# Performance work log

Measured on AMD Instinct MI355X. Metric: run time of the kernel, lower is better.

The kernel has to match this reference:

```python
import jax, jax.numpy as jnp
import numpy as np

EPS = 1e-5
S = 192  # seq_len = 24*8
D = 512
DFF = 2048


def setup_inputs() -> dict:
    key = jax.random.key(0)
    ks = jax.random.split(key, 8)
    tgt = jax.random.normal(ks[0], (64, 24, 8, D), jnp.float32)
    memory = jax.random.normal(ks[1], (64, 24, 8, D), jnp.float32)
    W1 = jax.random.normal(ks[2], (D, D), jnp.float32) * 0.02
    b1 = jnp.zeros((D,), jnp.float32)
    se = jax.random.normal(ks[3], (S, S), jnp.float32)
    score_embed = (se + se.T).reshape(1, 1, S, S)
    W2 = jax.random.normal(ks[4], (DFF, S), jnp.float32) * 0.05
    b2 = jnp.zeros((DFF,), jnp.float32)
    W3 = jax.random.normal(ks[5], (1, DFF), jnp.float32) * 0.02
    b3 = jnp.zeros((1,), jnp.float32)
    return {
        'tgt': tgt, 'memory': memory,
        'W1': W1, 'b1': b1, 'score_embed': score_embed,
        'g1': jnp.ones((1,), jnp.float32), 'be1': jnp.zeros((1,), jnp.float32),
        'W2': W2, 'b2': b2,
        'g2': jnp.ones((DFF,), jnp.float32), 'be2': jnp.zeros((DFF,), jnp.float32),
        'W3': W3, 'b3': b3,
        'g3': jnp.ones((1,), jnp.float32), 'be3': jnp.zeros((1,), jnp.float32),
    }


def _bn(x, gamma, beta, axes):
    # BatchNorm in training mode: biased variance over `axes`.
    mean = jnp.mean(x, axis=axes, keepdims=True)
    var = jnp.mean((x - mean) ** 2, axis=axes, keepdims=True)
    return gamma * (x - mean) * jax.lax.rsqrt(var + EPS) + beta


def reference(tgt, memory, W1, b1, score_embed, g1, be1, W2, b2, g2, be2, W3, b3, g3, be3):
    q = tgt.shape[0]
    k = memory.shape[0]
    d = tgt.shape[-1]
    tgt = tgt.reshape(q, S, d)      # [q, t, d]
    memory = memory.reshape(k, S, d)  # [k, s, d]
    query = tgt @ W1.T + b1
    key = memory @ W1.T + b1
    # bilinear score with learned symmetric bias: [q, k, s, t]
    score = jnp.einsum('qtd,ksd->qkst', query, key) * jax.nn.sigmoid(score_embed)
    score = score.reshape(q * k, S, S)
    # dual-axis max pooling, concat -> [q*k, 2S]
    score = jnp.concatenate((score.max(axis=1), score.max(axis=2)), axis=-1)
    x = score.reshape(-1, 1, S)                       # [2qk, 1, S]
    x = _bn(x, g1.reshape(1, 1, 1), be1.reshape(1, 1, 1), (0, 2)).reshape(-1, S)
    x = x @ W2.T + b2                                 # [2qk, DFF]
    x = _bn(x, g2, be2, (0,))
    x = jax.nn.relu(x)
    x = x @ W3.T + b3                                 # [2qk, 1]
    x = x.reshape(-1, 2).sum(axis=-1, keepdims=True)  # [qk, 1]
    x = _bn(x, g3, be3, (0,))
    return x.reshape(q, k)
```

## Files before the change

kernel.cpp:

```cpp
#include <hip/hip_runtime.h>

#define SS 192
#define DD 512
#define DFF 2048
#define NROW 12288
#define EPSV 1e-5f

using bf16x8 = __attribute__((ext_vector_type(8))) __bf16;
using f32x4  = __attribute__((ext_vector_type(4))) float;

__device__ inline unsigned short f2bf(float f) {
    unsigned u = __float_as_uint(f);
    unsigned r = (u + 0x7FFFu + ((u >> 16) & 1u)) >> 16;
    return (unsigned short)r;
}
__device__ inline float bf2f(unsigned short h) {
    return __uint_as_float(((unsigned)h) << 16);
}
__device__ inline unsigned f2mono(float f) {
    unsigned u = __float_as_uint(f);
    return u ^ ((unsigned)((int)u >> 31) | 0x80000000u);
}
__device__ inline float mono2f(unsigned u) {
    unsigned b = (u & 0x80000000u) ? (u ^ 0x80000000u) : ~u;
    return __uint_as_float(b);
}
#define ENC_NEGINF 0x007FFFFFu

#define GLL16(g, l) __builtin_amdgcn_global_load_lds( \
    (const __attribute__((address_space(1))) void*)(g), \
    (__attribute__((address_space(3))) void*)(l), 16, 0, 0)

template<int NW>
__device__ inline float blockReduceSum(float v) {
    __shared__ float red[NW];
    #pragma unroll
    for (int o = 32; o > 0; o >>= 1) v += __shfl_down(v, o);
    int w = threadIdx.x >> 6;
    __syncthreads();
    if ((threadIdx.x & 63) == 0) red[w] = v;
    __syncthreads();
    if (threadIdx.x == 0) {
        float t = 0;
        #pragma unroll
        for (int i = 0; i < NW; i++) t += red[i];
        red[0] = t;
    }
    __syncthreads();
    return red[0];
}

__global__ void k_cvt(const float* __restrict__ src, unsigned short* __restrict__ dst) {
    int i = blockIdx.x * 256 + threadIdx.x;
    float4 v = ((const float4*)src)[i];
    unsigned short o[4] = { f2bf(v.x), f2bf(v.y), f2bf(v.z), f2bf(v.w) };
    ((uint2*)dst)[i] = *(uint2*)o;
}

__global__ void k_sig(const float* __restrict__ se, float* __restrict__ sig) {
    int i = blockIdx.x * 256 + threadIdx.x;
    sig[i] = 1.0f / (1.0f + __expf(-se[i]));
}

__global__ void k_rowsum(const float* __restrict__ W2, float* __restrict__ rowsum) {
    int f = blockIdx.x * 256 + threadIdx.x;
    float s = 0.f;
    for (int i = 0; i < SS; i++) s += W2[(size_t)f * SS + i];
    rowsum[f] = s;
}

__global__ __launch_bounds__(256) void k_proj(
    const unsigned short* __restrict__ xbf, const unsigned short* __restrict__ w1bf,
    const float* __restrict__ b1, unsigned short* __restrict__ outQK)
{
    __shared__ unsigned short sA[3][128 * 32];
    __shared__ unsigned short sB[3][128 * 32];
    const int tid = threadIdx.x;
    const int lane = tid & 63;
    const int w = tid >> 6;
    const int m0 = blockIdx.x * 128;
    const int n0 = blockIdx.y * 128;
    const int wm = (w >> 1) * 64, wn = (w & 1) * 64;

    f32x4 acc[4][4] = {};

    const int sr  = lane >> 2;
    const int scg = (lane & 3) ^ ((lane >> 3) & 3);
    const unsigned short* Ab = xbf  + (size_t)m0 * DD;
    const unsigned short* Bb = w1bf + (size_t)n0 * DD;
    const unsigned short* AsrcB = Ab + (size_t)(w * 2 * 16 + sr) * DD + scg * 8;
    const unsigned short* BsrcB = Bb + (size_t)(w * 2 * 16 + sr) * DD + scg * 8;

    const int l16 = lane & 15, g = lane >> 4;
    const int cswz = ((g ^ ((l16 >> 1) & 3))) * 8;

    #pragma unroll
    for (int pt = 0; pt < 2; pt++) {
        #pragma unroll
        for (int i = 0; i < 2; i++) {
            int rb = w * 2 + i;
            GLL16(AsrcB + (size_t)i * 16 * DD + pt * 32, &sA[pt][rb * 512]);
            GLL16(BsrcB + (size_t)i * 16 * DD + pt * 32, &sB[pt][rb * 512]);
        }
    }

    #pragma unroll
    for (int t = 0; t < 16; t++) {
        if (t < 15) asm volatile("s_waitcnt vmcnt(4)" ::: "memory");
        else        asm volatile("s_waitcnt vmcnt(0)" ::: "memory");
        __builtin_amdgcn_s_barrier();
        if (t + 2 < 16) {
            const int buf = (t + 2) % 3;
            const int k0  = (t + 2) * 32;
            #pragma unroll
            for (int i = 0; i < 2; i++) {
                int rb = w * 2 + i;
                GLL16(AsrcB + (size_t)i * 16 * DD + k0, &sA[buf][rb * 512]);
                GLL16(BsrcB + (size_t)i * 16 * DD + k0, &sB[buf][rb * 512]);
            }
        }
        const int cur = t % 3;
        const unsigned short* aBase = &sA[cur][(wm + l16) * 32 + cswz];
        const unsigned short* bBase = &sB[cur][(wn + l16) * 32 + cswz];
        bf16x8 af[4];
        #pragma unroll
        for (int mi = 0; mi < 4; mi++) af[mi] = *(const bf16x8*)(aBase + mi * 512);
        __builtin_amdgcn_s_setprio(1);
        #pragma unroll
        for (int ni = 0; ni < 4; ni++) {
            bf16x8 bfr = *(const bf16x8*)(bBase + ni * 512);
            #pragma unroll
            for (int mi = 0; mi < 4; mi++)
                acc[mi][ni] = __builtin_amdgcn_mfma_f32_16x16x32_bf16(af[mi], bfr, acc[mi][ni], 0, 0, 0);
        }
        __builtin_amdgcn_s_setprio(0);
    }

    const int rg = lane >> 4;
    #pragma unroll
    for (int ni = 0; ni < 4; ni++) {
        int e = n0 + wn + ni * 16 + l16;
        float bias = b1[e];
        #pragma unroll
        for (int mi = 0; mi < 4; mi++) {
            #pragma unroll
            for (int r = 0; r < 4; r++) {
                int row = m0 + wm + mi * 16 + rg * 4 + r;
                outQK[(size_t)row * DD + e] = f2bf(acc[mi][ni][r] + bias);
            }
        }
    }
}

__global__ __launch_bounds__(512, 4) void k_score(
    const unsigned short* __restrict__ qB,
    const unsigned short* __restrict__ kB,
    const float* __restrict__ sig,
    float* __restrict__ pooled)
{
    __shared__ unsigned short sA[3][192 * 32];
    __shared__ unsigned short sB[3][192 * 32];
    __shared__ unsigned maxT[192];
    __shared__ unsigned maxS[192];

    const int tid = threadIdx.x;
    const int p = blockIdx.x;
    const int q = p >> 6, kk = p & 63;
    const unsigned short* Ab = kB + (size_t)kk * SS * DD;
    const unsigned short* Bb = qB + (size_t)q * SS * DD;

    if (tid < 192) { maxT[tid] = ENC_NEGINF; maxS[tid] = ENC_NEGINF; }

    const int lane = tid & 63, w = tid >> 6;
    const int wsr = (w >> 2) * 96;
    const int wtc = (w & 3) * 48;

    f32x4 acc[6][3] = {};

    const int sr  = lane >> 2;
    const int scg = (lane & 3) ^ ((lane >> 3) & 3);
    const bool isA = (w < 4);
    const int wg = (isA ? w : (w - 4)) * 3;
    const unsigned short* srcB = (isA ? Ab : Bb) + (size_t)(wg * 16 + sr) * DD + scg * 8;
    unsigned short* dst0 = isA ? &sA[0][0] : &sB[0][0];

    const int l16 = lane & 15, g = lane >> 4;
    const int cswz = ((g ^ ((l16 >> 1) & 3))) * 8;

    #pragma unroll
    for (int pt = 0; pt < 2; pt++) {
        #pragma unroll
        for (int i = 0; i < 3; i++)
            GLL16(srcB + (size_t)i * 16 * DD + pt * 32, dst0 + pt * (192 * 32) + (wg + i) * 512);
    }

    #pragma unroll
    for (int t = 0; t < 16; t++) {
        if (t < 15) asm volatile("s_waitcnt vmcnt(3)" ::: "memory");
        else        asm volatile("s_waitcnt vmcnt(0)" ::: "memory");
        __builtin_amdgcn_s_barrier();
        if (t + 2 < 16) {
            const int buf = (t + 2) % 3;
            const int k0  = (t + 2) * 32;
            #pragma unroll
            for (int i = 0; i < 3; i++)
                GLL16(srcB + (size_t)i * 16 * DD + k0, dst0 + buf * (192 * 32) + (wg + i) * 512);
        }
        const int cur = t % 3;
        const unsigned short* aBase = &sA[cur][(wsr + l16) * 32 + cswz];
        const unsigned short* bBase = &sB[cur][(wtc + l16) * 32 + cswz];
        bf16x8 af[6];
        #pragma unroll
        for (int mi = 0; mi < 6; mi++) af[mi] = *(const bf16x8*)(aBase + mi * 512);
        __builtin_amdgcn_s_setprio(1);
        #pragma unroll
        for (int ni = 0; ni < 3; ni++) {
            bf16x8 bfr = *(const bf16x8*)(bBase + ni * 512);
            #pragma unroll
            for (int mi = 0; mi < 6; mi++)
                acc[mi][ni] = __builtin_amdgcn_mfma_f32_16x16x32_bf16(af[mi], bfr, acc[mi][ni], 0, 0, 0);
        }
        __builtin_amdgcn_s_setprio(0);
    }

    const int rg = lane >> 4;

    #pragma unroll
    for (int mi = 0; mi < 6; mi++) {
        #pragma unroll
        for (int r = 0; r < 4; r++) {
            int s = wsr + mi * 16 + rg * 4 + r;
            const float* srow = sig + (size_t)s * SS + wtc;
            #pragma unroll
            for (int ni = 0; ni < 3; ni++)
                acc[mi][ni][r] *= srow[ni * 16 + l16];
        }
    }

    #pragma unroll
    for (int ni = 0; ni < 3; ni++) {
        float cm = -INFINITY;
        #pragma unroll
        for (int mi = 0; mi < 6; mi++)
            #pragma unroll
            for (int r = 0; r < 4; r++)
                cm = fmaxf(cm, acc[mi][ni][r]);
        cm = fmaxf(cm, __shfl_xor(cm, 16));
        cm = fmaxf(cm, __shfl_xor(cm, 32));
        if (lane < 16) atomicMax(&maxT[wtc + ni * 16 + lane], f2mono(cm));
    }
    #pragma unroll
    for (int mi = 0; mi < 6; mi++) {
        #pragma unroll
        for (int r = 0; r < 4; r++) {
            float rm = -INFINITY;
            #pragma unroll
            for (int ni = 0; ni < 3; ni++) rm = fmaxf(rm, acc[mi][ni][r]);
            rm = fmaxf(rm, __shfl_xor(rm, 1));
            rm = fmaxf(rm, __shfl_xor(rm, 2));
            rm = fmaxf(rm, __shfl_xor(rm, 4));
            rm = fmaxf(rm, __shfl_xor(rm, 8));
            if ((lane & 15) == 0)
                atomicMax(&maxS[wsr + mi * 16 + rg * 4 + r], f2mono(rm));
        }
    }
    __syncthreads();
    float* out = pooled + (size_t)p * 384;
    if (tid < 192) {
        out[tid]       = mono2f(maxT[tid]);
        out[192 + tid] = mono2f(maxS[tid]);
    }
}

__global__ __launch_bounds__(256) void k_bn1(const float* __restrict__ pooled, float* __restrict__ bn1) {
    float s = 0.f, ss = 0.f;
    size_t base = (size_t)blockIdx.x * 8192;
    for (int i = 0; i < 32; i++) {
        float v = pooled[base + i * 256 + threadIdx.x];
        s += v; ss += v * v;
    }
    s  = blockReduceSum<4>(s);
    ss = blockReduceSum<4>(ss);
    if (threadIdx.x == 0) { atomicAdd(&bn1[0], s); atomicAdd(&bn1[1], ss); }
}

__global__ __launch_bounds__(256) void k_w2(
    const float* __restrict__ x, const float* __restrict__ W2,
    const float* __restrict__ b2, const float* __restrict__ rowsum,
    const float* __restrict__ bn1, const float* __restrict__ g1,
    const float* __restrict__ be1, unsigned short* __restrict__ z)
{
    __shared__ unsigned short lA[128][40];
    __shared__ unsigned short lB[128][40];
    const int tid = threadIdx.x;
    const int lane = tid & 63;
    const int w = tid >> 6;
    const int m0 = blockIdx.x * 128;
    const int n0 = blockIdx.y * 128;
    const int wm = (w >> 1) * 64, wn = (w & 1) * 64;

    f32x4 acc[4][4] = {};
    const int srow = tid >> 1;
    const int scol = (tid & 1) * 16;
    const float* Asrc = x  + (size_t)(m0 + srow) * SS;
    const float* Bsrc = W2 + (size_t)(n0 + srow) * SS;

    for (int k0 = 0; k0 < SS; k0 += 32) {
        {
            unsigned short tmp[16];
            const float4* s4 = (const float4*)(Asrc + k0 + scol);
            #pragma unroll
            for (int i = 0; i < 4; i++) {
                float4 v = s4[i];
                tmp[i*4+0] = f2bf(v.x); tmp[i*4+1] = f2bf(v.y);
                tmp[i*4+2] = f2bf(v.z); tmp[i*4+3] = f2bf(v.w);
            }
            *(uint4*)(&lA[srow][scol])     = *(uint4*)(&tmp[0]);
            *(uint4*)(&lA[srow][scol + 8]) = *(uint4*)(&tmp[8]);
            const float4* t4 = (const float4*)(Bsrc + k0 + scol);
            #pragma unroll
            for (int i = 0; i < 4; i++) {
                float4 v = t4[i];
                tmp[i*4+0] = f2bf(v.x); tmp[i*4+1] = f2bf(v.y);
                tmp[i*4+2] = f2bf(v.z); tmp[i*4+3] = f2bf(v.w);
            }
            *(uint4*)(&lB[srow][scol])     = *(uint4*)(&tmp[0]);
            *(uint4*)(&lB[srow][scol + 8]) = *(uint4*)(&tmp[8]);
        }
        __syncthreads();
        const int l16 = lane & 15, kg = (lane >> 4) * 8;
        bf16x8 af[4];
        #pragma unroll
        for (int mi = 0; mi < 4; mi++)
            af[mi] = *(const bf16x8*)(&lA[wm + mi*16 + l16][kg]);
        #pragma unroll
        for (int ni = 0; ni < 4; ni++) {
            bf16x8 bfr = *(const bf16x8*)(&lB[wn + ni*16 + l16][kg]);
            #pragma unroll
            for (int mi = 0; mi < 4; mi++)
                acc[mi][ni] = __builtin_amdgcn_mfma_f32_16x16x32_bf16(af[mi], bfr, acc[mi][ni], 0, 0, 0);
        }
        __syncthreads();
    }

    const float n1 = 8192.0f * 192.0f;
    const float m1 = bn1[0] / n1;
    const float v1 = bn1[1] / n1 - m1 * m1;
    const float a1 = g1[0] * rsqrtf(v1 + EPSV);
    const float c1 = be1[0] - m1 * a1;

    const int l16 = lane & 15, rg = lane >> 4;
    #pragma unroll
    for (int ni = 0; ni < 4; ni++) {
        int f = n0 + wn + ni*16 + l16;
        float add = c1 * rowsum[f] + b2[f];
        #pragma unroll
        for (int mi = 0; mi < 4; mi++) {
            #pragma unroll
            for (int r = 0; r < 4; r++) {
                int row = m0 + wm + mi*16 + rg*4 + r;
                z[(size_t)row * DFF + f] = f2bf(a1 * acc[mi][ni][r] + add);
            }
        }
    }
}

__global__ __launch_bounds__(256) void k_colstat(
    const unsigned short* __restrict__ z, float* __restrict__ cs, float* __restrict__ css)
{
    int c0 = threadIdx.x * 8;
    size_t r0 = (size_t)blockIdx.x * 256;
    float s[8] = {}, ss[8] = {};
    for (int i = 0; i < 256; i++) {
        uint4 v = *(const uint4*)(z + (r0 + i) * DFF + c0);
        unsigned short pv[8];
        *(uint4*)pv = v;
        #pragma unroll
        for (int j = 0; j < 8; j++) { float x = bf2f(pv[j]); s[j] += x; ss[j] += x * x; }
    }
    #pragma unroll
    for (int j = 0; j < 8; j++) {
        atomicAdd(&cs[c0 + j], s[j]);
        atomicAdd(&css[c0 + j], ss[j]);
    }
}

__global__ void k_coef(const float* __restrict__ cs, const float* __restrict__ css,
                       const float* __restrict__ g2, const float* __restrict__ be2,
                       float* __restrict__ a2, float* __restrict__ c2)
{
    int f = blockIdx.x * 256 + threadIdx.x;
    float m  = cs[f] * (1.0f / 8192.0f);
    float vr = css[f] * (1.0f / 8192.0f) - m * m;
    float a  = g2[f] * rsqrtf(vr + EPSV);
    a2[f] = a;
    c2[f] = be2[f] - m * a;
}

__global__ __launch_bounds__(256) void k_final_dot(
    const unsigned short* __restrict__ z, const float* __restrict__ a2,
    const float* __restrict__ c2, const float* __restrict__ W3,
    const float* __restrict__ b3, float* __restrict__ rowout)
{
    const int lane = threadIdx.x & 63, w = threadIdx.x >> 6;
    float4 av[4][2], cv[4][2], wv[4][2];
    #pragma unroll
    for (int c = 0; c < 4; c++) {
        int col = c * 512 + lane * 8;
        av[c][0] = *(const float4*)(a2 + col); av[c][1] = *(const float4*)(a2 + col + 4);
        cv[c][0] = *(const float4*)(c2 + col); cv[c][1] = *(const float4*)(c2 + col + 4);
        wv[c][0] = *(const float4*)(W3 + col); wv[c][1] = *(const float4*)(W3 + col + 4);
    }
    const float bias = b3[0];
    int r0 = blockIdx.x * 16 + w * 4;
    #pragma unroll
    for (int rr = 0; rr < 4; rr++) {
        int row = r0 + rr;
        float sum = 0.f;
        #pragma unroll
        for (int c = 0; c < 4; c++) {
            uint4 v = *(const uint4*)(z + (size_t)row * DFF + c * 512 + lane * 8);
            unsigned short pv[8];
            *(uint4*)pv = v;
            #pragma unroll
            for (int j = 0; j < 8; j++) {
                float a = ((const float*)&av[c][j >> 2])[j & 3];
                float cc = ((const float*)&cv[c][j >> 2])[j & 3];
                float wf = ((const float*)&wv[c][j >> 2])[j & 3];
                float x = a * bf2f(pv[j]) + cc;
                sum += fmaxf(x, 0.f) * wf;
            }
        }
        #pragma unroll
        for (int o = 32; o > 0; o >>= 1) sum += __shfl_down(sum, o);
        if (lane == 0) rowout[row] = sum + bias;
    }
}

__global__ __launch_bounds__(1024) void k_out(
    const float* __restrict__ rowout, const float* __restrict__ g3,
    const float* __restrict__ be3, float* __restrict__ out)
{
    float pv0, pv1, pv2, pv3;
    float s = 0.f, ss = 0.f;
    {
        int p0 = threadIdx.x;
        pv0 = rowout[2*p0] + rowout[2*p0+1];
        int p1 = 1024 + threadIdx.x;
        pv1 = rowout[2*p1] + rowout[2*p1+1];
        int p2 = 2048 + threadIdx.x;
        pv2 = rowout[2*p2] + rowout[2*p2+1];
        int p3 = 3072 + threadIdx.x;
        pv3 = rowout[2*p3] + rowout[2*p3+1];
        s = pv0 + pv1 + pv2 + pv3;
        ss = pv0*pv0 + pv1*pv1 + pv2*pv2 + pv3*pv3;
    }
    s  = blockReduceSum<16>(s);
    ss = blockReduceSum<16>(ss);
    float m  = s * (1.0f / 4096.0f);
    float vr = ss * (1.0f / 4096.0f) - m * m;
    float a  = g3[0] * rsqrtf(vr + EPSV);
    float c  = be3[0] - m * a;
    out[threadIdx.x]        = a * pv0 + c;
    out[1024 + threadIdx.x] = a * pv1 + c;
    out[2048 + threadIdx.x] = a * pv2 + c;
    out[3072 + threadIdx.x] = a * pv3 + c;
}

extern "C" void kernel_launch(void* const* d_in, const int* in_sizes, int n_in,
                              void* d_out, int out_size, void* d_ws, size_t ws_size,
                              hipStream_t stream)
{
    const float* tgt = (const float*)d_in[0];
    const float* mem = (const float*)d_in[1];
    const float* W1  = (const float*)d_in[2];
    const float* b1  = (const float*)d_in[3];
    const float* se  = (const float*)d_in[4];
    const float* g1  = (const float*)d_in[5];
    const float* be1 = (const float*)d_in[6];
    const float* W2  = (const float*)d_in[7];
    const float* b2  = (const float*)d_in[8];
    const float* g2  = (const float*)d_in[9];
    const float* be2 = (const float*)d_in[10];
    const float* W3  = (const float*)d_in[11];
    const float* b3  = (const float*)d_in[12];
    const float* g3  = (const float*)d_in[13];
    const float* be3 = (const float*)d_in[14];
    float* out = (float*)d_out;

    char* ws = (char*)d_ws;
    size_t off = 0;
    auto alloc = [&](size_t bytes) { void* p = ws + off; off += (bytes + 255) & ~(size_t)255; return p; };

    char* region0 = (char*)alloc((size_t)8192 * DFF * 2);
    unsigned short* xbf = (unsigned short*)region0;
    unsigned short* z   = (unsigned short*)region0;
    unsigned short* qk  = (unsigned short*)alloc((size_t)24576 * DD * 2);
    unsigned short* w1bf= (unsigned short*)alloc((size_t)DD * DD * 2);
    float* sig          = (float*)alloc((size_t)SS * SS * 4);
    float* pooled       = (float*)alloc((size_t)4096 * 384 * 4);
    float* rowsum       = (float*)alloc(DFF * 4);
    float* stats        = (float*)alloc((2 + 2 * DFF) * 4);
    float* a2           = (float*)alloc(DFF * 4);
    float* c2           = (float*)alloc(DFF * 4);
    float* rowout       = (float*)alloc(8192 * 4);

    float* bn1 = stats;
    float* cs  = stats + 2;
    float* css = stats + 2 + DFF;

    hipMemsetAsync(stats, 0, (2 + 2 * DFF) * 4, stream);

    k_cvt<<<6144, 256, 0, stream>>>(tgt, xbf);
    k_cvt<<<6144, 256, 0, stream>>>(mem, xbf + (size_t)NROW * DD);
    k_cvt<<<256,  256, 0, stream>>>(W1, w1bf);
    k_sig<<<144, 256, 0, stream>>>(se, sig);
    k_rowsum<<<8, 256, 0, stream>>>(W2, rowsum);
    k_proj<<<dim3(192, 4), 256, 0, stream>>>(xbf, w1bf, b1, qk);
    k_score<<<4096, 512, 0, stream>>>(qk, qk + (size_t)NROW * DD, sig, pooled);
    k_bn1<<<192, 256, 0, stream>>>(pooled, bn1);
    k_w2<<<dim3(64, 16), 256, 0, stream>>>(pooled, W2, b2, rowsum, bn1, g1, be1, z);
    k_colstat<<<32, 256, 0, stream>>>(z, cs, css);
    k_coef<<<8, 256, 0, stream>>>(cs, css, g2, be2, a2, c2);
    k_final_dot<<<512, 256, 0, stream>>>(z, a2, c2, W3, b3, rowout);
    k_out<<<1, 1024, 0, stream>>>(rowout, g3, be3, out);
}
```

Baseline: 353.5 us.

## Fuse BN statistics into score and W2 epilogues, retile score warps

Folds the BN1 sum/sum-of-squares reduction into the score kernel epilogue and the BN2 column statistics into the W2 GEMM epilogue, and computes the BN2 coefficients inside the final dot kernel. This removes three launches and a full re-read of z and of pooled. It also changes the score kernel warp tiling from a 2x4 grid (96x48 per warp) to a 4x2 grid (48x96 per warp). The catch is many more atomics on global and shared memory, and column statistics now come from fp32 values rather than the rounded bf16 values of z.

```diff
diff --git a/kernel.cpp b/kernel.cpp
--- a/kernel.cpp
+++ b/kernel.cpp
@@ -156,7 +156,8 @@
     const unsigned short* __restrict__ qB,
     const unsigned short* __restrict__ kB,
     const float* __restrict__ sig,
-    float* __restrict__ pooled)
+    float* __restrict__ pooled,
+    float* __restrict__ bn1)
 {
     __shared__ unsigned short sA[3][192 * 32];
     __shared__ unsigned short sB[3][192 * 32];
@@ -172,10 +173,10 @@
     if (tid < 192) { maxT[tid] = ENC_NEGINF; maxS[tid] = ENC_NEGINF; }
 
     const int lane = tid & 63, w = tid >> 6;
-    const int wsr = (w >> 2) * 96;
-    const int wtc = (w & 3) * 48;
-
-    f32x4 acc[6][3] = {};
+    const int wsr = (w >> 1) * 48;
+    const int wtc = (w & 1) * 96;
+
+    f32x4 acc[3][6] = {};
 
     const int sr  = lane >> 2;
     const int scg = (lane & 3) ^ ((lane >> 3) & 3);
@@ -209,15 +210,15 @@
         const int cur = t % 3;
         const unsigned short* aBase = &sA[cur][(wsr + l16) * 32 + cswz];
         const unsigned short* bBase = &sB[cur][(wtc + l16) * 32 + cswz];
-        bf16x8 af[6];
-        #pragma unroll
-        for (int mi = 0; mi < 6; mi++) af[mi] = *(const bf16x8*)(aBase + mi * 512);
+        bf16x8 af[3];
+        #pragma unroll
+        for (int mi = 0; mi < 3; mi++) af[mi] = *(const bf16x8*)(aBase + mi * 512);
         __builtin_amdgcn_s_setprio(1);
         #pragma unroll
-        for (int ni = 0; ni < 3; ni++) {
+        for (int ni = 0; ni < 6; ni++) {
             bf16x8 bfr = *(const bf16x8*)(bBase + ni * 512);
             #pragma unroll
-            for (int mi = 0; mi < 6; mi++)
+            for (int mi = 0; mi < 3; mi++)
                 acc[mi][ni] = __builtin_amdgcn_mfma_f32_16x16x32_bf16(af[mi], bfr, acc[mi][ni], 0, 0, 0);
         }
         __builtin_amdgcn_s_setprio(0);
@@ -226,22 +227,22 @@
     const int rg = lane >> 4;
 
     #pragma unroll
-    for (int mi = 0; mi < 6; mi++) {
+    for (int mi = 0; mi < 3; mi++) {
         #pragma unroll
         for (int r = 0; r < 4; r++) {
             int s = wsr + mi * 16 + rg * 4 + r;
             const float* srow = sig + (size_t)s * SS + wtc;
             #pragma unroll
-            for (int ni = 0; ni < 3; ni++)
+            for (int ni = 0; ni < 6; ni++)
                 acc[mi][ni][r] *= srow[ni * 16 + l16];
         }
     }
 
     #pragma unroll
-    for (int ni = 0; ni < 3; ni++) {
+    for (int ni = 0; ni < 6; ni++) {
         float cm = -INFINITY;
         #pragma unroll
-        for (int mi = 0; mi < 6; mi++)
+        for (int mi = 0; mi < 3; mi++)
             #pragma unroll
             for (int r = 0; r < 4; r++)
                 cm = fmaxf(cm, acc[mi][ni][r]);
@@ -250,12 +251,12 @@
         if (lane < 16) atomicMax(&maxT[wtc + ni * 16 + lane], f2mono(cm));
     }
     #pragma unroll
-    for (int mi = 0; mi < 6; mi++) {
+    for (int mi = 0; mi < 3; mi++) {
         #pragma unroll
         for (int r = 0; r < 4; r++) {
             float rm = -INFINITY;
             #pragma unroll
-            for (int ni = 0; ni < 3; ni++) rm = fmaxf(rm, acc[mi][ni][r]);
+            for (int ni = 0; ni < 6; ni++) rm = fmaxf(rm, acc[mi][ni][r]);
             rm = fmaxf(rm, __shfl_xor(rm, 1));
             rm = fmaxf(rm, __shfl_xor(rm, 2));
             rm = fmaxf(rm, __shfl_xor(rm, 4));
@@ -266,29 +267,24 @@
     }
     __syncthreads();
     float* out = pooled + (size_t)p * 384;
+    float v1 = 0.f, v2 = 0.f;
     if (tid < 192) {
-        out[tid]       = mono2f(maxT[tid]);
-        out[192 + tid] = mono2f(maxS[tid]);
-    }
-}
-
-__global__ __launch_bounds__(256) void k_bn1(const float* __restrict__ pooled, float* __restrict__ bn1) {
-    float s = 0.f, ss = 0.f;
-    size_t base = (size_t)blockIdx.x * 8192;
-    for (int i = 0; i < 32; i++) {
-        float v = pooled[base + i * 256 + threadIdx.x];
-        s += v; ss += v * v;
-    }
-    s  = blockReduceSum<4>(s);
-    ss = blockReduceSum<4>(ss);
-    if (threadIdx.x == 0) { atomicAdd(&bn1[0], s); atomicAdd(&bn1[1], ss); }
+        v1 = mono2f(maxT[tid]);
+        v2 = mono2f(maxS[tid]);
+        out[tid]       = v1;
+        out[192 + tid] = v2;
+    }
+    float ps  = blockReduceSum<8>(v1 + v2);
+    float pss = blockReduceSum<8>(v1 * v1 + v2 * v2);
+    if (tid == 0) { atomicAdd(&bn1[0], ps); atomicAdd(&bn1[1], pss); }
 }
 
 __global__ __launch_bounds__(256) void k_w2(
     const float* __restrict__ x, const float* __restrict__ W2,
     const float* __restrict__ b2, const float* __restrict__ rowsum,
     const float* __restrict__ bn1, const float* __restrict__ g1,
-    const float* __restrict__ be1, unsigned short* __restrict__ z)
+    const float* __restrict__ be1, unsigned short* __restrict__ z,
+    float* __restrict__ cs, float* __restrict__ css)
 {
     __shared__ unsigned short lA[128][40];
     __shared__ unsigned short lB[128][40];
@@ -349,57 +345,42 @@
     const float a1 = g1[0] * rsqrtf(v1 + EPSV);
     const float c1 = be1[0] - m1 * a1;
 
+    float* colsum = (float*)&lA[0][0];
+    float* colssq = colsum + 128;
+    if (tid < 128) { colsum[tid] = 0.f; colssq[tid] = 0.f; }
+    __syncthreads();
+
     const int l16 = lane & 15, rg = lane >> 4;
     #pragma unroll
     for (int ni = 0; ni < 4; ni++) {
-        int f = n0 + wn + ni*16 + l16;
+        int lc = wn + ni*16 + l16;
+        int f = n0 + lc;
         float add = c1 * rowsum[f] + b2[f];
+        float s_ = 0.f, ss_ = 0.f;
         #pragma unroll
         for (int mi = 0; mi < 4; mi++) {
             #pragma unroll
             for (int r = 0; r < 4; r++) {
                 int row = m0 + wm + mi*16 + rg*4 + r;
-                z[(size_t)row * DFF + f] = f2bf(a1 * acc[mi][ni][r] + add);
-            }
-        }
-    }
-}
-
-__global__ __launch_bounds__(256) void k_colstat(
-    const unsigned short* __restrict__ z, float* __restrict__ cs, float* __restrict__ css)
-{
-    int c0 = threadIdx.x * 8;
-    size_t r0 = (size_t)blockIdx.x * 256;
-    float s[8] = {}, ss[8] = {};
-    for (int i = 0; i < 256; i++) {
-        uint4 v = *(const uint4*)(z + (r0 + i) * DFF + c0);
-        unsigned short pv[8];
-        *(uint4*)pv = v;
-        #pragma unroll
-        for (int j = 0; j < 8; j++) { float x = bf2f(pv[j]); s[j] += x; ss[j] += x * x; }
-    }
-    #pragma unroll
-    for (int j = 0; j < 8; j++) {
-        atomicAdd(&cs[c0 + j], s[j]);
-        atomicAdd(&css[c0 + j], ss[j]);
-    }
-}
-
-__global__ void k_coef(const float* __restrict__ cs, const float* __restrict__ css,
-                       const float* __restrict__ g2, const float* __restrict__ be2,
-                       float* __restrict__ a2, float* __restrict__ c2)
-{
-    int f = blockIdx.x * 256 + threadIdx.x;
-    float m  = cs[f] * (1.0f / 8192.0f);
-    float vr = css[f] * (1.0f / 8192.0f) - m * m;
-    float a  = g2[f] * rsqrtf(vr + EPSV);
-    a2[f] = a;
-    c2[f] = be2[f] - m * a;
+                float y = a1 * acc[mi][ni][r] + add;
+                z[(size_t)row * DFF + f] = f2bf(y);
+                s_ += y; ss_ += y * y;
+            }
+        }
+        atomicAdd(&colsum[lc], s_);
+        atomicAdd(&colssq[lc], ss_);
+    }
+    __syncthreads();
+    if (tid < 128) {
+        atomicAdd(&cs[n0 + tid],  colsum[tid]);
+        atomicAdd(&css[n0 + tid], colssq[tid]);
+    }
 }
 
 __global__ __launch_bounds__(256) void k_final_dot(
-    const unsigned short* __restrict__ z, const float* __restrict__ a2,
-    const float* __restrict__ c2, const float* __restrict__ W3,
+    const unsigned short* __restrict__ z, const float* __restrict__ cs,
+    const float* __restrict__ css, const float* __restrict__ g2,
+    const float* __restrict__ be2, const float* __restrict__ W3,
     const float* __restrict__ b3, float* __restrict__ rowout)
 {
     const int lane = threadIdx.x & 63, w = threadIdx.x >> 6;
@@ -407,9 +388,25 @@
     #pragma unroll
     for (int c = 0; c < 4; c++) {
         int col = c * 512 + lane * 8;
-        av[c][0] = *(const float4*)(a2 + col); av[c][1] = *(const float4*)(a2 + col + 4);
-        cv[c][0] = *(const float4*)(c2 + col); cv[c][1] = *(const float4*)(c2 + col + 4);
-        wv[c][0] = *(const float4*)(W3 + col); wv[c][1] = *(const float4*)(W3 + col + 4);
+        #pragma unroll
+        for (int h = 0; h < 2; h++) {
+            float4 csv  = *(const float4*)(cs  + col + 4*h);
+            float4 cssv = *(const float4*)(css + col + 4*h);
+            float4 g2v  = *(const float4*)(g2  + col + 4*h);
+            float4 be2v = *(const float4*)(be2 + col + 4*h);
+            wv[c][h]    = *(const float4*)(W3  + col + 4*h);
+            float* mp = (float*)&csv; float* sp = (float*)&cssv;
+            float* gp = (float*)&g2v; float* bp = (float*)&be2v;
+            float* ap = (float*)&av[c][h]; float* cp = (float*)&cv[c][h];
+            #pragma unroll
+            for (int j = 0; j < 4; j++) {
+                float m  = mp[j] * (1.0f / 8192.0f);
+                float vr = sp[j] * (1.0f / 8192.0f) - m * m;
+                float a  = gp[j] * rsqrtf(vr + EPSV);
+                ap[j] = a;
+                cp[j] = bp[j] - m * a;
+            }
+        }
     }
     const float bias = b3[0];
     int r0 = blockIdx.x * 16 + w * 4;
@@ -501,8 +498,6 @@
     float* pooled       = (float*)alloc((size_t)4096 * 384 * 4);
     float* rowsum       = (float*)alloc(DFF * 4);
     float* stats        = (float*)alloc((2 + 2 * DFF) * 4);
-    float* a2           = (float*)alloc(DFF * 4);
-    float* c2           = (float*)alloc(DFF * 4);
     float* rowout       = (float*)alloc(8192 * 4);
 
     float* bn1 = stats;
@@ -517,11 +512,8 @@
     k_sig<<<144, 256, 0, stream>>>(se, sig);
     k_rowsum<<<8, 256, 0, stream>>>(W2, rowsum);
     k_proj<<<dim3(192, 4), 256, 0, stream>>>(xbf, w1bf, b1, qk);
-    k_score<<<4096, 512, 0, stream>>>(qk, qk + (size_t)NROW * DD, sig, pooled);
-    k_bn1<<<192, 256, 0, stream>>>(pooled, bn1);
-    k_w2<<<dim3(64, 16), 256, 0, stream>>>(pooled, W2, b2, rowsum, bn1, g1, be1, z);
-    k_colstat<<<32, 256, 0, stream>>>(z, cs, css);
-    k_coef<<<8, 256, 0, stream>>>(cs, css, g2, be2, a2, c2);
-    k_final_dot<<<512, 256, 0, stream>>>(z, a2, c2, W3, b3, rowout);
+    k_score<<<4096, 512, 0, stream>>>(qk, qk + (size_t)NROW * DD, sig, pooled, bn1);
+    k_w2<<<dim3(64, 16), 256, 0, stream>>>(pooled, W2, b2, rowsum, bn1, g1, be1, z, cs, css);
+    k_final_dot<<<512, 256, 0, stream>>>(z, cs, css, g2, be2, W3, b3, rowout);
     k_out<<<1, 1024, 0, stream>>>(rowout, g3, be3, out);
 }
```

New measurement: 369.1 us. 1.04x slower.
